# Kernel optimization log

Measured on AMD Instinct MI355X. Metric: run time of the kernel, lower is better.

Reference implementation:

```python
import jax, jax.numpy as jnp
import numpy as np

IN_DIM = 8192
OUT_DIM = 4096
NNZ = 1638400
BATCH = 4096


def setup_inputs() -> dict:
    key = jax.random.key(0)
    k_x, k_r, k_c, k_w = jax.random.split(key, 4)
    x = jax.random.normal(k_x, (BATCH, IN_DIM), dtype=jnp.float32)
    row_idx = jax.random.randint(k_r, (NNZ,), 0, IN_DIM, dtype=jnp.int64)
    col_idx = jax.random.randint(k_c, (NNZ,), 0, OUT_DIM, dtype=jnp.int64)
    # xavier_uniform on a [nnz, 1] tensor: bound = sqrt(6 / (nnz + 1))
    bound = float(np.sqrt(6.0 / (NNZ + 1)))
    weights = jax.random.uniform(k_w, (NNZ,), dtype=jnp.float32, minval=-bound, maxval=bound)
    bias = jnp.zeros((OUT_DIM,), dtype=jnp.float32)
    return {"x": x, "row_idx": row_idx, "col_idx": col_idx, "weights": weights, "bias": bias}


def reference(x, row_idx, col_idx, weights, bias):
    # scatter_nd: build dense [IN_DIM, OUT_DIM] weight matrix via scatter-add
    ind1d = row_idx * OUT_DIM + col_idx  # flat indices, duplicates accumulate
    W = jnp.zeros((IN_DIM * OUT_DIM,), dtype=weights.dtype).at[ind1d].add(weights)
    W = W.reshape(IN_DIM, OUT_DIM)
    # dense matmul + bias, matching torch.mm(x, sparse_tensor) + bias
    return x @ W + bias
```

## Files before the change

### kernel.cpp

```cpp
#include <hip/hip_runtime.h>
#include <stdint.h>

#define IN_DIM 8192
#define OUT_DIM 4096
#define NNZ 1638400
#define BATCH 4096

typedef __bf16 bf16x8 __attribute__((ext_vector_type(8)));
typedef float f32x4 __attribute__((ext_vector_type(4)));
typedef short s16x2 __attribute__((ext_vector_type(2)));


__device__ __forceinline__ unsigned short f2bf(float f) {
  union { float f; unsigned int u; } v; v.f = f;
  unsigned int u = v.u;
  unsigned int r = (u + 0x7FFFu + ((u >> 16) & 1u)) >> 16;
  return (unsigned short)r;
}

__device__ __forceinline__ float bf2f(unsigned short b) {
  union { unsigned int u; float f; } v;
  v.u = (unsigned int)b << 16;
  return v.f;
}

__device__ __forceinline__ void async16(const void* g, void* l) {
  __builtin_amdgcn_global_load_lds(
      (const __attribute__((address_space(1))) unsigned int*)g,
      (__attribute__((address_space(3))) unsigned int*)l,
      16, 0, 0);
}

__device__ __forceinline__ void convert_body(int i, const float* __restrict__ src,
                                             unsigned short* __restrict__ dst) {
  const float4* s = (const float4*)src;
  float4 a = s[2 * i];
  float4 b = s[2 * i + 1];
  union { unsigned short us[8]; uint4 v; } o;
  o.us[0] = f2bf(a.x); o.us[1] = f2bf(a.y); o.us[2] = f2bf(a.z); o.us[3] = f2bf(a.w);
  o.us[4] = f2bf(b.x); o.us[5] = f2bf(b.y); o.us[6] = f2bf(b.z); o.us[7] = f2bf(b.w);
  ((uint4*)dst)[i] = o.v;
}


#define PREP_BLOCKS ((IN_DIM * OUT_DIM) / 8 / 256)

__global__ void prep_kernel(uint4* __restrict__ W_zero,
                            const float* __restrict__ x,
                            unsigned short* __restrict__ x_bf16) {
  int i = blockIdx.x * 256 + threadIdx.x;
  W_zero[i] = make_uint4(0, 0, 0, 0);
  convert_body(i, x, x_bf16);
}


#if defined(__has_builtin)
#  if __has_builtin(__builtin_amdgcn_global_atomic_fadd_v2bf16)
#    define HAVE_PK_BF16 1
#  endif
#endif

__device__ __forceinline__ void scat1(int c, int r, float w,
                                      unsigned int* __restrict__ W) {
  size_t e = (size_t)c * IN_DIM + r;
  const bool hi = (e & 1);
  unsigned short nb = f2bf(w);
#ifdef HAVE_PK_BF16
  s16x2 v;
  v.x = hi ? (short)0 : (short)nb;
  v.y = hi ? (short)nb : (short)0;
  __builtin_amdgcn_global_atomic_fadd_v2bf16(
      (__attribute__((address_space(1))) s16x2*)(W + (e >> 1)), v);
#else
  unsigned int* p = W + (e >> 1);
  unsigned int nw0 = hi ? ((unsigned int)nb << 16) : (unsigned int)nb;
  unsigned int cur = atomicCAS(p, 0u, nw0);
  if (cur == 0u) return;
  unsigned int assumed;
  do {
    assumed = cur;
    unsigned short h = hi ? (unsigned short)(assumed >> 16)
                          : (unsigned short)(assumed & 0xFFFFu);
    unsigned short b2 = f2bf(bf2f(h) + w);
    unsigned int nw = hi ? ((assumed & 0x0000FFFFu) | ((unsigned int)b2 << 16))
                         : ((assumed & 0xFFFF0000u) | (unsigned int)b2);
    cur = atomicCAS(p, assumed, nw);
  } while (cur != assumed);
#endif
}

#define SCAT_BLOCKS (NNZ / 4 / 256)

__global__ void scatter_kernel(const int4* __restrict__ ri4,
                               const int4* __restrict__ ci4,
                               const float4* __restrict__ w4,
                               unsigned int* __restrict__ W) {
  int i = blockIdx.x * 256 + threadIdx.x;
  int4 r = ri4[i];
  int4 c = ci4[i];
  float4 w = w4[i];
  scat1(c.x, r.x, w.x, W);
  scat1(c.y, r.y, w.y, W);
  scat1(c.z, r.z, w.z, W);
  scat1(c.w, r.w, w.w, W);
}


#define TBM 256
#define TBN 256
#define TBK 64
#define NKT (IN_DIM / TBK)

__global__ __launch_bounds__(512, 2) void gemm_kernel(
    const unsigned short* __restrict__ A,
    const unsigned short* __restrict__ Bt,
    const float* __restrict__ bias,
    float* __restrict__ C) {
  extern __shared__ __align__(16) unsigned short lds[];

  const int tid = threadIdx.x;

  const int bid = blockIdx.x;
  const int swz = ((bid & 7) << 5) | (bid >> 3);
  const int m0 = (swz & 15) * TBM;
  const int n0 = (swz >> 4) * TBN;

  const int wid = tid >> 6;
  const int lane = tid & 63;
  const int wm = wid >> 2;
  const int wn = wid & 3;
  const int quad = lane >> 4;
  const int lm = lane & 15;
  const int xorv = lm & 7;

  const unsigned short* Ab = A + (size_t)m0 * IN_DIM;
  const unsigned short* Bb = Bt + (size_t)n0 * IN_DIM;

  int soff[4], ldst[4];
#pragma unroll
  for (int c = 0; c < 4; ++c) {
    const int t2 = c * 512 + tid;
    const int srow = t2 >> 3;
    const int sseg = (t2 & 7) ^ (srow & 7);
    soff[c] = srow * IN_DIM + sseg * 8;
    ldst[c] = t2 * 16;
  }

  f32x4 acc[8][4] = {};

#define STAGE(kt_, b_, c_)                                                  \
  do {                                                                      \
    const int k0_ = (kt_)*TBK;                                              \
    char* la_ = (char*)lds + (b_)*65536;                                    \
    async16(Ab + (size_t)soff[c_] + k0_, la_ + ldst[c_]);                   \
    async16(Bb + (size_t)soff[c_] + k0_, la_ + 32768 + ldst[c_]);           \
  } while (0)

#pragma unroll
  for (int c = 0; c < 4; ++c) STAGE(0, 0, c);

  for (int kt = 0; kt < NKT; ++kt) {
    const int buf = kt & 1;
    const int nbuf = buf ^ 1;
    const int ktn = (kt + 1) & (NKT - 1);

    STAGE(ktn, nbuf, 0);
    asm volatile("s_waitcnt vmcnt(2)" ::: "memory");
    __builtin_amdgcn_sched_barrier(0);
    __builtin_amdgcn_s_barrier();

    const unsigned short* lA = lds + buf * 32768;
    const unsigned short* lB = lA + 16384;

    bf16x8 bfr[4][2];
#pragma unroll
    for (int j = 0; j < 4; ++j) {
      const int row = wn * 64 + j * 16 + lm;
#pragma unroll
      for (int ss = 0; ss < 2; ++ss) {
        const int p = ((ss << 2) | quad) ^ xorv;
        bfr[j][ss] = *(const bf16x8*)(lB + row * TBK + p * 8);
      }
    }

#pragma unroll
    for (int q = 0; q < 4; ++q) {
      bf16x8 af[2][2];
#pragma unroll
      for (int i = 0; i < 2; ++i) {
        const int row = wm * 128 + (q * 2 + i) * 16 + lm;
#pragma unroll
        for (int ss = 0; ss < 2; ++ss) {
          const int p = ((ss << 2) | quad) ^ xorv;
          af[i][ss] = *(const bf16x8*)(lA + row * TBK + p * 8);
        }
      }
      if (q < 3) STAGE(ktn, nbuf, q + 1);
      __builtin_amdgcn_s_barrier();
      __builtin_amdgcn_s_setprio(1);
#pragma unroll
      for (int i = 0; i < 2; ++i)
#pragma unroll
        for (int j = 0; j < 4; ++j)
#pragma unroll
          for (int ss = 0; ss < 2; ++ss)
            acc[q * 2 + i][j] = __builtin_amdgcn_mfma_f32_16x16x32_bf16(
                af[i][ss], bfr[j][ss], acc[q * 2 + i][j], 0, 0, 0);
      __builtin_amdgcn_s_setprio(0);
      __builtin_amdgcn_s_barrier();
    }
  }
#undef STAGE

  const int ccol0 = n0 + wn * 64 + lm;
  const int crow0 = m0 + wm * 128;
#pragma unroll
  for (int j = 0; j < 4; ++j) {
    const int col = ccol0 + j * 16;
    const float bv = bias[col];
#pragma unroll
    for (int i = 0; i < 8; ++i) {
#pragma unroll
      for (int v = 0; v < 4; ++v) {
        const int row = crow0 + i * 16 + quad * 4 + v;
        C[(size_t)row * OUT_DIM + col] = acc[i][j][v] + bv;
      }
    }
  }
}


extern "C" void kernel_launch(void* const* d_in, const int* in_sizes, int n_in,
                              void* d_out, int out_size, void* d_ws, size_t ws_size,
                              hipStream_t stream) {
  const float* x = (const float*)d_in[0];
  const int* row_idx = (const int*)d_in[1];
  const int* col_idx = (const int*)d_in[2];
  const float* weights = (const float*)d_in[3];
  const float* bias = (const float*)d_in[4];
  float* out = (float*)d_out;

  const size_t W_BF16_BYTES = (size_t)IN_DIM * OUT_DIM * 2;
  unsigned short* W_bf16 = (unsigned short*)d_ws;
  unsigned short* x_bf16 = (unsigned short*)((char*)d_ws + W_BF16_BYTES);

  static bool attr_set = false;
  if (!attr_set) {
    (void)hipFuncSetAttribute((const void*)gemm_kernel,
                              hipFuncAttributeMaxDynamicSharedMemorySize,
                              131072);
    attr_set = true;
  }

  prep_kernel<<<PREP_BLOCKS, 256, 0, stream>>>((uint4*)W_bf16, x, x_bf16);

  scatter_kernel<<<SCAT_BLOCKS, 256, 0, stream>>>(
      (const int4*)row_idx, (const int4*)col_idx, (const float4*)weights,
      (unsigned int*)W_bf16);

  gemm_kernel<<<dim3(256), dim3(512), 131072, stream>>>(x_bf16, W_bf16, bias, out);
}
```

Before: 522.8 us.

## Prefetch next B fragments into registers and move x conversion into scatter kernel

The GEMM main loop is restructured so the B-tile register fragments for the next k-step are read from LDS one step early, using two ping-pong fragment sets and a 2x unrolled k-loop. Global-to-LDS staging is split into separate A and B phases interleaved across the four MFMA quarters. Separately, the x fp32-to-bf16 conversion moves from the zeroing kernel into the scatter kernel, so zeroing becomes a pure store kernel. The B prefetch raises register pressure, and the vmcnt(0) wait at each step may stall the pipeline.

```diff
diff --git a/kernel.cpp b/kernel.cpp
--- a/kernel.cpp
+++ b/kernel.cpp
@@ -16,12 +16,6 @@
   unsigned int u = v.u;
   unsigned int r = (u + 0x7FFFu + ((u >> 16) & 1u)) >> 16;
   return (unsigned short)r;
-}
-
-__device__ __forceinline__ float bf2f(unsigned short b) {
-  union { unsigned int u; float f; } v;
-  v.u = (unsigned int)b << 16;
-  return v.f;
 }
 
 __device__ __forceinline__ void async16(const void* g, void* l) {
@@ -43,14 +37,10 @@
 }
 
 
-#define PREP_BLOCKS ((IN_DIM * OUT_DIM) / 8 / 256)
-
-__global__ void prep_kernel(uint4* __restrict__ W_zero,
-                            const float* __restrict__ x,
-                            unsigned short* __restrict__ x_bf16) {
-  int i = blockIdx.x * 256 + threadIdx.x;
-  W_zero[i] = make_uint4(0, 0, 0, 0);
-  convert_body(i, x, x_bf16);
+#define ZERO_BLOCKS ((IN_DIM * OUT_DIM) / 8 / 256)
+
+__global__ void zero_kernel(uint4* __restrict__ W) {
+  W[blockIdx.x * 256 + threadIdx.x] = make_uint4(0, 0, 0, 0);
 }
 
 
@@ -81,7 +71,8 @@
     assumed = cur;
     unsigned short h = hi ? (unsigned short)(assumed >> 16)
                           : (unsigned short)(assumed & 0xFFFFu);
-    unsigned short b2 = f2bf(bf2f(h) + w);
+    union { unsigned int u; float f; } hv; hv.u = (unsigned int)h << 16;
+    unsigned short b2 = f2bf(hv.f + w);
     unsigned int nw = hi ? ((assumed & 0x0000FFFFu) | ((unsigned int)b2 << 16))
                          : ((assumed & 0xFFFF0000u) | (unsigned int)b2);
     cur = atomicCAS(p, assumed, nw);
@@ -89,20 +80,23 @@
 #endif
 }
 
-#define SCAT_BLOCKS (NNZ / 4 / 256)
-
-__global__ void scatter_kernel(const int4* __restrict__ ri4,
-                               const int4* __restrict__ ci4,
-                               const float4* __restrict__ w4,
-                               unsigned int* __restrict__ W) {
+__global__ void conv_scat_kernel(const float* __restrict__ x,
+                                 unsigned short* __restrict__ x_bf16,
+                                 const int4* __restrict__ ri4,
+                                 const int4* __restrict__ ci4,
+                                 const float4* __restrict__ w4,
+                                 unsigned int* __restrict__ W) {
   int i = blockIdx.x * 256 + threadIdx.x;
-  int4 r = ri4[i];
-  int4 c = ci4[i];
-  float4 w = w4[i];
-  scat1(c.x, r.x, w.x, W);
-  scat1(c.y, r.y, w.y, W);
-  scat1(c.z, r.z, w.z, W);
-  scat1(c.w, r.w, w.w, W);
+  convert_body(i, x, x_bf16);
+  if (i < NNZ / 4) {
+    int4 r = ri4[i];
+    int4 c = ci4[i];
+    float4 w = w4[i];
+    scat1(c.x, r.x, w.x, W);
+    scat1(c.y, r.y, w.y, W);
+    scat1(c.z, r.z, w.z, W);
+    scat1(c.w, r.w, w.w, W);
+  }
 }
 
 
@@ -148,69 +142,106 @@
 
   f32x4 acc[8][4] = {};
 
-#define STAGE(kt_, b_, c_)                                                  \
-  do {                                                                      \
-    const int k0_ = (kt_)*TBK;                                              \
-    char* la_ = (char*)lds + (b_)*65536;                                    \
-    async16(Ab + (size_t)soff[c_] + k0_, la_ + ldst[c_]);                   \
-    async16(Bb + (size_t)soff[c_] + k0_, la_ + 32768 + ldst[c_]);           \
-  } while (0)
-
-#pragma unroll
-  for (int c = 0; c < 4; ++c) STAGE(0, 0, c);
-
-  for (int kt = 0; kt < NKT; ++kt) {
-    const int buf = kt & 1;
-    const int nbuf = buf ^ 1;
-    const int ktn = (kt + 1) & (NKT - 1);
-
-    STAGE(ktn, nbuf, 0);
-    asm volatile("s_waitcnt vmcnt(2)" ::: "memory");
-    __builtin_amdgcn_sched_barrier(0);
-    __builtin_amdgcn_s_barrier();
-
-    const unsigned short* lA = lds + buf * 32768;
-    const unsigned short* lB = lA + 16384;
-
-    bf16x8 bfr[4][2];
-#pragma unroll
-    for (int j = 0; j < 4; ++j) {
-      const int row = wn * 64 + j * 16 + lm;
-#pragma unroll
-      for (int ss = 0; ss < 2; ++ss) {
-        const int p = ((ss << 2) | quad) ^ xorv;
-        bfr[j][ss] = *(const bf16x8*)(lB + row * TBK + p * 8);
-      }
-    }
-
-#pragma unroll
-    for (int q = 0; q < 4; ++q) {
-      bf16x8 af[2][2];
-#pragma unroll
-      for (int i = 0; i < 2; ++i) {
-        const int row = wm * 128 + (q * 2 + i) * 16 + lm;
-#pragma unroll
-        for (int ss = 0; ss < 2; ++ss) {
-          const int p = ((ss << 2) | quad) ^ xorv;
-          af[i][ss] = *(const bf16x8*)(lA + row * TBK + p * 8);
-        }
-      }
-      if (q < 3) STAGE(ktn, nbuf, q + 1);
-      __builtin_amdgcn_s_barrier();
-      __builtin_amdgcn_s_setprio(1);
-#pragma unroll
-      for (int i = 0; i < 2; ++i)
-#pragma unroll
-        for (int j = 0; j < 4; ++j)
-#pragma unroll
-          for (int ss = 0; ss < 2; ++ss)
-            acc[q * 2 + i][j] = __builtin_amdgcn_mfma_f32_16x16x32_bf16(
-                af[i][ss], bfr[j][ss], acc[q * 2 + i][j], 0, 0, 0);
-      __builtin_amdgcn_s_setprio(0);
-      __builtin_amdgcn_s_barrier();
-    }
-  }
-#undef STAGE
+#define STAGE_A(kt_, b_, c_)                                                   \
+  async16(Ab + (size_t)soff[c_] + (kt_)*TBK,                                   \
+          (char*)lds + (b_)*65536 + ldst[c_])
+#define STAGE_B(kt_, b_, c_)                                                   \
+  async16(Bb + (size_t)soff[c_] + (kt_)*TBK,                                   \
+          (char*)lds + (b_)*65536 + 32768 + ldst[c_])
+
+#define RD_AF(lA_, q_)                                                         \
+  do {                                                                         \
+    _Pragma("unroll") for (int i = 0; i < 2; ++i) {                            \
+      const int row = wm * 128 + ((q_)*2 + i) * 16 + lm;                       \
+      _Pragma("unroll") for (int ss = 0; ss < 2; ++ss) {                       \
+        const int p = ((ss << 2) | quad) ^ xorv;                               \
+        af[i][ss] = *(const bf16x8*)((lA_) + row * TBK + p * 8);               \
+      }                                                                        \
+    }                                                                          \
+  } while (0)
+
+#define RD_BF(lB_, BFR)                                                        \
+  do {                                                                         \
+    _Pragma("unroll") for (int j = 0; j < 4; ++j) {                            \
+      const int row = wn * 64 + j * 16 + lm;                                   \
+      _Pragma("unroll") for (int ss = 0; ss < 2; ++ss) {                       \
+        const int p = ((ss << 2) | quad) ^ xorv;                               \
+        BFR[j][ss] = *(const bf16x8*)((lB_) + row * TBK + p * 8);              \
+      }                                                                        \
+    }                                                                          \
+  } while (0)
+
+#define MFMA_Q(q_, BFR)                                                        \
+  do {                                                                         \
+    __builtin_amdgcn_s_setprio(1);                                             \
+    _Pragma("unroll") for (int i = 0; i < 2; ++i)                              \
+    _Pragma("unroll") for (int j = 0; j < 4; ++j)                              \
+    _Pragma("unroll") for (int ss = 0; ss < 2; ++ss)                           \
+      acc[(q_)*2 + i][j] = __builtin_amdgcn_mfma_f32_16x16x32_bf16(            \
+          af[i][ss], BFR[j][ss], acc[(q_)*2 + i][j], 0, 0, 0);                 \
+    __builtin_amdgcn_s_setprio(0);                                             \
+  } while (0)
+
+#define KT_BODY(kt_, buf_, BFRC, BFRN)                                         \
+  do {                                                                         \
+    const int nxt_ = (buf_) ^ 1;                                               \
+    const int ktn_ = ((kt_) + 1) & (NKT - 1);                                  \
+    const unsigned short* lA_ = lds + (buf_)*32768;                            \
+    const unsigned short* lBn_ = lds + nxt_*32768 + 16384;                     \
+    bf16x8 af[2][2];                                                           \
+                           \
+    asm volatile("s_waitcnt vmcnt(0)" ::: "memory");                           \
+    __builtin_amdgcn_sched_barrier(0);                                         \
+    __builtin_amdgcn_s_barrier();                                              \
+    RD_AF(lA_, 0);                                                             \
+    STAGE_B(ktn_, nxt_, 0); STAGE_B(ktn_, nxt_, 1);                            \
+    __builtin_amdgcn_s_barrier();                                              \
+    MFMA_Q(0, BFRC);                                                           \
+    __builtin_amdgcn_s_barrier();                                              \
+                                                                  \
+    RD_AF(lA_, 1);                                                             \
+    STAGE_B(ktn_, nxt_, 2); STAGE_B(ktn_, nxt_, 3);                            \
+    __builtin_amdgcn_s_barrier();                                              \
+    MFMA_Q(1, BFRC);                                                           \
+    __builtin_amdgcn_s_barrier();                                              \
+                                                                  \
+    RD_AF(lA_, 2);                                                             \
+    STAGE_A(ktn_, nxt_, 0); STAGE_A(ktn_, nxt_, 1);                            \
+    __builtin_amdgcn_s_barrier();                                              \
+    MFMA_Q(2, BFRC);                                                           \
+    __builtin_amdgcn_s_barrier();                                              \
+           \
+    asm volatile("s_waitcnt vmcnt(2)" ::: "memory");                           \
+    __builtin_amdgcn_sched_barrier(0);                                         \
+    __builtin_amdgcn_s_barrier();                                              \
+    RD_AF(lA_, 3);                                                             \
+    RD_BF(lBn_, BFRN);                                                         \
+    STAGE_A(ktn_, nxt_, 2); STAGE_A(ktn_, nxt_, 3);                            \
+    __builtin_amdgcn_s_barrier();                                              \
+    MFMA_Q(3, BFRC);                                                           \
+  } while (0)
+
+#pragma unroll
+  for (int c = 0; c < 4; ++c) STAGE_B(0, 0, c);
+#pragma unroll
+  for (int c = 0; c < 4; ++c) STAGE_A(0, 0, c);
+  asm volatile("s_waitcnt vmcnt(4)" ::: "memory");
+  __builtin_amdgcn_sched_barrier(0);
+  __builtin_amdgcn_s_barrier();
+  bf16x8 bfrP[4][2], bfrQ[4][2];
+  RD_BF(lds + 16384, bfrP);
+
+  for (int kt = 0; kt < NKT; kt += 2) {
+    KT_BODY(kt, 0, bfrP, bfrQ);
+    KT_BODY(kt + 1, 1, bfrQ, bfrP);
+  }
+
+#undef KT_BODY
+#undef MFMA_Q
+#undef RD_BF
+#undef RD_AF
+#undef STAGE_B
+#undef STAGE_A
 
   const int ccol0 = n0 + wn * 64 + lm;
   const int crow0 = m0 + wm * 128;
@@ -252,11 +283,11 @@
     attr_set = true;
   }
 
-  prep_kernel<<<PREP_BLOCKS, 256, 0, stream>>>((uint4*)W_bf16, x, x_bf16);
-
-  scatter_kernel<<<SCAT_BLOCKS, 256, 0, stream>>>(
-      (const int4*)row_idx, (const int4*)col_idx, (const float4*)weights,
-      (unsigned int*)W_bf16);
+  zero_kernel<<<ZERO_BLOCKS, 256, 0, stream>>>((uint4*)W_bf16);
+
+  conv_scat_kernel<<<ZERO_BLOCKS, 256, 0, stream>>>(
+      x, x_bf16, (const int4*)row_idx, (const int4*)col_idx,
+      (const float4*)weights, (unsigned int*)W_bf16);
 
   gemm_kernel<<<dim3(256), dim3(512), 131072, stream>>>(x_bf16, W_bf16, bias, out);
 }
```

New measurement: 545.1 us. 4.3% more time.

## Fuse x conversion into scatter kernel and batch gemm prefetch loads

Applied to the files above, without the earlier changes.

Moves the fp32-to-bf16 conversion of x out of the zeroing kernel and into the scatter kernel, so the zero pass only writes and the scatter launch also does the conversion. In the GEMM main loop, all four async LDS prefetch loads for the next k-tile are now issued at the start of the iteration instead of being interleaved between MFMA sub-steps, and a final vmcnt(0) wait is added. This simplifies the schedule but may reduce overlap of global loads with compute and add contention at the top of each iteration.

```diff
diff --git a/kernel.cpp b/kernel.cpp
--- a/kernel.cpp
+++ b/kernel.cpp
@@ -16,12 +16,6 @@
   unsigned int u = v.u;
   unsigned int r = (u + 0x7FFFu + ((u >> 16) & 1u)) >> 16;
   return (unsigned short)r;
-}
-
-__device__ __forceinline__ float bf2f(unsigned short b) {
-  union { unsigned int u; float f; } v;
-  v.u = (unsigned int)b << 16;
-  return v.f;
 }
 
 __device__ __forceinline__ void async16(const void* g, void* l) {
@@ -43,14 +37,10 @@
 }
 
 
-#define PREP_BLOCKS ((IN_DIM * OUT_DIM) / 8 / 256)
-
-__global__ void prep_kernel(uint4* __restrict__ W_zero,
-                            const float* __restrict__ x,
-                            unsigned short* __restrict__ x_bf16) {
-  int i = blockIdx.x * 256 + threadIdx.x;
-  W_zero[i] = make_uint4(0, 0, 0, 0);
-  convert_body(i, x, x_bf16);
+#define ZERO_BLOCKS ((IN_DIM * OUT_DIM) / 8 / 256)
+
+__global__ void zero_kernel(uint4* __restrict__ W) {
+  W[blockIdx.x * 256 + threadIdx.x] = make_uint4(0, 0, 0, 0);
 }
 
 
@@ -81,7 +71,8 @@
     assumed = cur;
     unsigned short h = hi ? (unsigned short)(assumed >> 16)
                           : (unsigned short)(assumed & 0xFFFFu);
-    unsigned short b2 = f2bf(bf2f(h) + w);
+    union { unsigned int u; float f; } hv; hv.u = (unsigned int)h << 16;
+    unsigned short b2 = f2bf(hv.f + w);
     unsigned int nw = hi ? ((assumed & 0x0000FFFFu) | ((unsigned int)b2 << 16))
                          : ((assumed & 0xFFFF0000u) | (unsigned int)b2);
     cur = atomicCAS(p, assumed, nw);
@@ -89,20 +80,23 @@
 #endif
 }
 
-#define SCAT_BLOCKS (NNZ / 4 / 256)
-
-__global__ void scatter_kernel(const int4* __restrict__ ri4,
-                               const int4* __restrict__ ci4,
-                               const float4* __restrict__ w4,
-                               unsigned int* __restrict__ W) {
+__global__ void conv_scat_kernel(const float* __restrict__ x,
+                                 unsigned short* __restrict__ x_bf16,
+                                 const int4* __restrict__ ri4,
+                                 const int4* __restrict__ ci4,
+                                 const float4* __restrict__ w4,
+                                 unsigned int* __restrict__ W) {
   int i = blockIdx.x * 256 + threadIdx.x;
-  int4 r = ri4[i];
-  int4 c = ci4[i];
-  float4 w = w4[i];
-  scat1(c.x, r.x, w.x, W);
-  scat1(c.y, r.y, w.y, W);
-  scat1(c.z, r.z, w.z, W);
-  scat1(c.w, r.w, w.w, W);
+  convert_body(i, x, x_bf16);
+  if (i < NNZ / 4) {
+    int4 r = ri4[i];
+    int4 c = ci4[i];
+    float4 w = w4[i];
+    scat1(c.x, r.x, w.x, W);
+    scat1(c.y, r.y, w.y, W);
+    scat1(c.z, r.z, w.z, W);
+    scat1(c.w, r.w, w.w, W);
+  }
 }
 
 
@@ -141,8 +135,8 @@
   for (int c = 0; c < 4; ++c) {
     const int t2 = c * 512 + tid;
     const int srow = t2 >> 3;
-    const int sseg = (t2 & 7) ^ (srow & 7);
-    soff[c] = srow * IN_DIM + sseg * 8;
+    const int sgs = (t2 & 7) ^ (srow & 7);
+    soff[c] = srow * IN_DIM + sgs * 8;
     ldst[c] = t2 * 16;
   }
 
@@ -164,8 +158,9 @@
     const int nbuf = buf ^ 1;
     const int ktn = (kt + 1) & (NKT - 1);
 
-    STAGE(ktn, nbuf, 0);
-    asm volatile("s_waitcnt vmcnt(2)" ::: "memory");
+#pragma unroll
+    for (int c = 0; c < 4; ++c) STAGE(ktn, nbuf, c);
+    asm volatile("s_waitcnt vmcnt(8)" ::: "memory");
     __builtin_amdgcn_sched_barrier(0);
     __builtin_amdgcn_s_barrier();
 
@@ -195,7 +190,6 @@
           af[i][ss] = *(const bf16x8*)(lA + row * TBK + p * 8);
         }
       }
-      if (q < 3) STAGE(ktn, nbuf, q + 1);
       __builtin_amdgcn_s_barrier();
       __builtin_amdgcn_s_setprio(1);
 #pragma unroll
@@ -211,6 +205,8 @@
     }
   }
 #undef STAGE
+
+  asm volatile("s_waitcnt vmcnt(0)" ::: "memory");
 
   const int ccol0 = n0 + wn * 64 + lm;
   const int crow0 = m0 + wm * 128;
@@ -252,11 +248,11 @@
     attr_set = true;
   }
 
-  prep_kernel<<<PREP_BLOCKS, 256, 0, stream>>>((uint4*)W_bf16, x, x_bf16);
-
-  scatter_kernel<<<SCAT_BLOCKS, 256, 0, stream>>>(
-      (const int4*)row_idx, (const int4*)col_idx, (const float4*)weights,
-      (unsigned int*)W_bf16);
+  zero_kernel<<<ZERO_BLOCKS, 256, 0, stream>>>((uint4*)W_bf16);
+
+  conv_scat_kernel<<<ZERO_BLOCKS, 256, 0, stream>>>(
+      x, x_bf16, (const int4*)row_idx, (const int4*)col_idx,
+      (const float4*)weights, (unsigned int*)W_bf16);
 
   gemm_kernel<<<dim3(256), dim3(512), 131072, stream>>>(x_bf16, W_bf16, bias, out);
 }
```

New measurement: 562.9 us. 7.7% more time.

## Batch GEMM prefetch stages after one barrier and use CAS loop for scatter

Applied to the files above, without the earlier changes.

The GEMM main loop now waits for all outstanding global-to-LDS loads, takes a single barrier, and then issues all four prefetch chunks for the next K tile at once. This drops the per-quarter barriers and the staggered STAGE calls interleaved with the MFMA blocks, cutting sync overhead at the cost of a less finely interleaved load/compute schedule. The scatter step no longer uses the packed bf16 atomic add. It always does a plain read followed by a CAS retry loop, which may be slower under contention if the hardware atomic was in use before.

```diff
diff --git a/kernel.cpp b/kernel.cpp
--- a/kernel.cpp
+++ b/kernel.cpp
@@ -8,7 +8,6 @@
 
 typedef __bf16 bf16x8 __attribute__((ext_vector_type(8)));
 typedef float f32x4 __attribute__((ext_vector_type(4)));
-typedef short s16x2 __attribute__((ext_vector_type(2)));
 
 
 __device__ __forceinline__ unsigned short f2bf(float f) {
@@ -54,39 +53,22 @@
 }
 
 
-#if defined(__has_builtin)
-#  if __has_builtin(__builtin_amdgcn_global_atomic_fadd_v2bf16)
-#    define HAVE_PK_BF16 1
-#  endif
-#endif
-
 __device__ __forceinline__ void scat1(int c, int r, float w,
                                       unsigned int* __restrict__ W) {
   size_t e = (size_t)c * IN_DIM + r;
+  unsigned int* p = W + (e >> 1);
   const bool hi = (e & 1);
-  unsigned short nb = f2bf(w);
-#ifdef HAVE_PK_BF16
-  s16x2 v;
-  v.x = hi ? (short)0 : (short)nb;
-  v.y = hi ? (short)nb : (short)0;
-  __builtin_amdgcn_global_atomic_fadd_v2bf16(
-      (__attribute__((address_space(1))) s16x2*)(W + (e >> 1)), v);
-#else
-  unsigned int* p = W + (e >> 1);
-  unsigned int nw0 = hi ? ((unsigned int)nb << 16) : (unsigned int)nb;
-  unsigned int cur = atomicCAS(p, 0u, nw0);
-  if (cur == 0u) return;
+  unsigned int cur = *p;
   unsigned int assumed;
   do {
     assumed = cur;
     unsigned short h = hi ? (unsigned short)(assumed >> 16)
                           : (unsigned short)(assumed & 0xFFFFu);
-    unsigned short b2 = f2bf(bf2f(h) + w);
-    unsigned int nw = hi ? ((assumed & 0x0000FFFFu) | ((unsigned int)b2 << 16))
-                         : ((assumed & 0xFFFF0000u) | (unsigned int)b2);
+    unsigned short nb = f2bf(bf2f(h) + w);
+    unsigned int nw = hi ? ((assumed & 0x0000FFFFu) | ((unsigned int)nb << 16))
+                         : ((assumed & 0xFFFF0000u) | (unsigned int)nb);
     cur = atomicCAS(p, assumed, nw);
   } while (cur != assumed);
-#endif
 }
 
 #define SCAT_BLOCKS (NNZ / 4 / 256)
@@ -141,8 +123,8 @@
   for (int c = 0; c < 4; ++c) {
     const int t2 = c * 512 + tid;
     const int srow = t2 >> 3;
-    const int sseg = (t2 & 7) ^ (srow & 7);
-    soff[c] = srow * IN_DIM + sseg * 8;
+    const int sgs = (t2 & 7) ^ (srow & 7);
+    soff[c] = srow * IN_DIM + sgs * 8;
     ldst[c] = t2 * 16;
   }
 
@@ -164,10 +146,13 @@
     const int nbuf = buf ^ 1;
     const int ktn = (kt + 1) & (NKT - 1);
 
-    STAGE(ktn, nbuf, 0);
-    asm volatile("s_waitcnt vmcnt(2)" ::: "memory");
+    asm volatile("s_waitcnt vmcnt(0)" ::: "memory");
     __builtin_amdgcn_sched_barrier(0);
     __builtin_amdgcn_s_barrier();
+    __builtin_amdgcn_sched_barrier(0);
+
+#pragma unroll
+    for (int c = 0; c < 4; ++c) STAGE(ktn, nbuf, c);
 
     const unsigned short* lA = lds + buf * 32768;
     const unsigned short* lB = lA + 16384;
@@ -195,8 +180,6 @@
           af[i][ss] = *(const bf16x8*)(lA + row * TBK + p * 8);
         }
       }
-      if (q < 3) STAGE(ktn, nbuf, q + 1);
-      __builtin_amdgcn_s_barrier();
       __builtin_amdgcn_s_setprio(1);
 #pragma unroll
       for (int i = 0; i < 2; ++i)
@@ -207,10 +190,11 @@
             acc[q * 2 + i][j] = __builtin_amdgcn_mfma_f32_16x16x32_bf16(
                 af[i][ss], bfr[j][ss], acc[q * 2 + i][j], 0, 0, 0);
       __builtin_amdgcn_s_setprio(0);
-      __builtin_amdgcn_s_barrier();
     }
   }
 #undef STAGE
+
+  asm volatile("s_waitcnt vmcnt(0)" ::: "memory");
 
   const int ccol0 = n0 + wn * 64 + lm;
   const int crow0 = m0 + wm * 128;
```

Result: faster. 510.4 us (-2.4%).
